# Optimization experiments

Hardware: AMD Instinct MI355X
Metric: run time of the kernel (lower is better)

Reference implementation:

```python
import jax, jax.numpy as jnp
import numpy as np


def _lstm_dir(xs, Wih, Whh, bih, bhh, reverse):
    # xs: [T, B, E]; torch LSTM gate order i, f, g, o
    B = xs.shape[1]
    H = Whh.shape[1]
    h0 = jnp.zeros((B, H), xs.dtype)
    c0 = jnp.zeros((B, H), xs.dtype)

    def step(carry, xt):
        h, c = carry
        g = xt @ Wih.T + h @ Whh.T + (bih + bhh)
        i, f, gg, o = jnp.split(g, 4, axis=-1)
        i = jax.nn.sigmoid(i)
        f = jax.nn.sigmoid(f)
        gg = jnp.tanh(gg)
        o = jax.nn.sigmoid(o)
        c_new = f * c + i * gg
        h_new = o * jnp.tanh(c_new)
        return (h_new, c_new), h_new

    _, hs = jax.lax.scan(step, (h0, c0), xs, reverse=reverse)
    return hs  # [T, B, H] time-aligned


def _forward(x, edge_index, emb_table, Wih_f, Whh_f, bih_f, bhh_f,
             Wih_b, Whh_b, bih_b, bhh_b, label_emb, ggc_weight,
             gru_Wih, gru_Whh, gru_bih, gru_bhh, proj_W, proj_b):
    # --- embedding (dropout is identity in eval) ---
    emb = emb_table[x]                       # [B, T, E]
    xs = jnp.transpose(emb, (1, 0, 2))       # [T, B, E]
    hf = _lstm_dir(xs, Wih_f, Whh_f, bih_f, bhh_f, reverse=False)
    hb = _lstm_dir(xs, Wih_b, Whh_b, bih_b, bhh_b, reverse=True)
    c = jnp.concatenate([hf, hb], axis=-1)   # [T, B, 2H]
    c = jnp.transpose(c, (1, 0, 2))          # [B, T, 2H]

    # --- label cosine similarity, summed over tokens ---
    eps = 1e-8
    cn = c / jnp.maximum(jnp.linalg.norm(c, axis=-1, keepdims=True), eps)
    ln = label_emb / jnp.maximum(jnp.linalg.norm(label_emb, axis=-1, keepdims=True), eps)
    ls = jnp.einsum('btd,ld->bl', cn, ln)    # [B, C] (sum over t folded in)

    # --- GatedGraphConv, 2 layers, aggr='add', edge_weight=None ---
    src, dst = edge_index[0], edge_index[1]
    N = ls.shape[0]
    h = ls
    for i in range(ggc_weight.shape[0]):
        m = h @ ggc_weight[i]                            # [N, C]
        m = jax.ops.segment_sum(m[src], dst, num_segments=N)  # gather + scatter-add
        # torch GRUCell: gates r, z, n
        gi = m @ gru_Wih.T + gru_bih
        gh = h @ gru_Whh.T + gru_bhh
        ir, iz, inn = jnp.split(gi, 3, axis=-1)
        hr, hz, hn = jnp.split(gh, 3, axis=-1)
        r = jax.nn.sigmoid(ir + hr)
        z = jax.nn.sigmoid(iz + hz)
        n = jnp.tanh(inn + r * hn)
        h = (1.0 - z) * n + z * h

    return h @ proj_W.T + proj_b             # [B, C]


def setup_inputs() -> dict:
    key = jax.random.key(0)
    ks = jax.random.split(key, 20)
    V, E, B, T, C, NE = 50000, 300, 2048, 64, 1024, 65536
    H = E
    s = 0.05
    inp = {
        'x': jax.random.randint(ks[0], (B, T), 0, V),
        'edge_index': jax.random.randint(ks[1], (2, NE), 0, B),
        'emb_table': jax.random.normal(ks[2], (V, E)) * s,
        'Wih_f': jax.random.normal(ks[3], (4 * H, E)) * s,
        'Whh_f': jax.random.normal(ks[4], (4 * H, H)) * s,
        'bih_f': jnp.zeros((4 * H,)),
        'bhh_f': jnp.zeros((4 * H,)),
        'Wih_b': jax.random.normal(ks[5], (4 * H, E)) * s,
        'Whh_b': jax.random.normal(ks[6], (4 * H, H)) * s,
        'bih_b': jnp.zeros((4 * H,)),
        'bhh_b': jnp.zeros((4 * H,)),
        'label_emb': jax.random.normal(ks[7], (C, 2 * H)) * s,
        'ggc_weight': jax.random.normal(ks[8], (2, C, C)) * (1.0 / np.sqrt(C)),
        'gru_Wih': jax.random.normal(ks[9], (3 * C, C)) * (1.0 / np.sqrt(C)),
        'gru_Whh': jax.random.normal(ks[10], (3 * C, C)) * (1.0 / np.sqrt(C)),
        'gru_bih': jnp.zeros((3 * C,)),
        'gru_bhh': jnp.zeros((3 * C,)),
        'proj_W': jax.random.normal(ks[11], (C, C)) * (1.0 / np.sqrt(C)),
        'proj_b': jnp.zeros((C,)),
    }
    return inp


def reference(x, edge_index, emb_table, Wih_f, Whh_f, bih_f, bhh_f,
              Wih_b, Whh_b, bih_b, bhh_b, label_emb, ggc_weight,
              gru_Wih, gru_Whh, gru_bih, gru_bhh, proj_W, proj_b):
    return _forward(x, edge_index, emb_table, Wih_f, Whh_f, bih_f, bhh_f,
                    Wih_b, Whh_b, bih_b, bhh_b, label_emb, ggc_weight,
                    gru_Wih, gru_Whh, gru_bih, gru_bhh, proj_W, proj_b)
```

## Files before the change

### kernel.cpp

```cpp
#include <hip/hip_runtime.h>
#include <hip/hip_bf16.h>
#include <stdint.h>

typedef __hip_bfloat16 bf16;
typedef __attribute__((ext_vector_type(8))) short frag16;
typedef __attribute__((ext_vector_type(4))) float f32x4;

#define B_ 2048
#define T_ 64
#define E_ 300
#define H_ 300
#define C_ 1024
#define NE_ 65536
#define HP 320
#define KC 640
#define NP 1280

static __device__ __forceinline__ float sigf(float x) {
  x = fminf(fmaxf(x, -30.f), 30.f);
  return 1.f / (1.f + __expf(-x));
}
static __device__ __forceinline__ float tanhfast(float x) {
  x = fminf(fmaxf(x, -15.f), 15.f);
  float e = __expf(2.f * x);
  return (e - 1.f) / (e + 1.f);
}
static __device__ __forceinline__ float ldraw(const void* p, size_t i, int isb) {
  return isb ? __bfloat162float(((const bf16*)p)[i]) : ((const float*)p)[i];
}
static __device__ __forceinline__ short b2s(bf16 b) {
  short s; __builtin_memcpy(&s, &b, 2); return s;
}
static __device__ __forceinline__ short4 f4tob4(float4 v) {
  return make_short4(b2s(__float2bfloat16(v.x)), b2s(__float2bfloat16(v.y)),
                     b2s(__float2bfloat16(v.z)), b2s(__float2bfloat16(v.w)));
}

__global__ void detect_dtype(const unsigned short* __restrict__ e2, int* __restrict__ flag) {
  __shared__ int red[4];
  int tid = threadIdx.x;
  int ones = 0;
#pragma unroll
  for (int s = 0; s < 16; ++s) ones += (e2[2 * (tid * 16 + s)] >> 14) & 1;
  for (int off = 32; off > 0; off >>= 1) ones += __shfl_down(ones, off, 64);
  if ((tid & 63) == 0) red[tid >> 6] = ones;
  __syncthreads();
  if (tid == 0) {
    int tot = red[0] + red[1] + red[2] + red[3];
    *flag = (tot < 1024) ? 1 : 0;
  }
}

__global__ __launch_bounds__(256) void gemm_bt(
    const bf16* __restrict__ A, int lda,
    const void* __restrict__ W, int ldw,
    const void* __restrict__ bias,
    float* __restrict__ Cf, bf16* __restrict__ Cb, int ldc, int K,
    const int* __restrict__ rawp, int outmode) {
  __shared__ __align__(16) short As[2][128 * 32];
  __shared__ __align__(16) short Bs[2][128 * 32];
  const int isb = rawp ? *rawp : 1;
  const int n0 = blockIdx.x * 128, m0 = blockIdx.y * 128;
  const int lane = threadIdx.x & 63, wv = threadIdx.x >> 6;
  const int wm = (wv & 1) * 64, wn = (wv >> 1) * 64;
  const int r_ = threadIdx.x >> 1, half_ = threadIdx.x & 1;
  const short* Arow = (const short*)A + (size_t)(m0 + r_) * lda + half_ * 16;
  const short* Brs = (const short*)W + (size_t)(n0 + r_) * ldw + half_ * 16;
  const float* Brf = (const float*)W + (size_t)(n0 + r_) * ldw + half_ * 16;

  uint4 ra0, ra1, rb0, rb1;
  float4 rf0, rf1, rf2, rf3;
  auto loadT = [&](int k0) {
    ra0 = *(const uint4*)(Arow + k0);
    ra1 = *(const uint4*)(Arow + k0 + 8);
    if (isb) {
      rb0 = *(const uint4*)(Brs + k0);
      rb1 = *(const uint4*)(Brs + k0 + 8);
    } else {
      rf0 = *(const float4*)(Brf + k0);
      rf1 = *(const float4*)(Brf + k0 + 4);
      rf2 = *(const float4*)(Brf + k0 + 8);
      rf3 = *(const float4*)(Brf + k0 + 12);
    }
  };
  auto writeT = [&](int buf) {
    short* da = As[buf] + r_ * 32 + half_ * 16;
    *(uint4*)da = ra0;
    *(uint4*)(da + 8) = ra1;
    short* db = Bs[buf] + r_ * 32 + half_ * 16;
    if (isb) {
      *(uint4*)db = rb0;
      *(uint4*)(db + 8) = rb1;
    } else {
      *(short4*)db = f4tob4(rf0);
      *(short4*)(db + 4) = f4tob4(rf1);
      *(short4*)(db + 8) = f4tob4(rf2);
      *(short4*)(db + 12) = f4tob4(rf3);
    }
  };

  f32x4 acc[4][4];
#pragma unroll
  for (int i = 0; i < 4; ++i)
#pragma unroll
    for (int j = 0; j < 4; ++j) acc[i][j] = (f32x4){0.f, 0.f, 0.f, 0.f};

  const int nk = K / 32;
  loadT(0);
  writeT(0);
  __syncthreads();
  const int krd = (lane >> 4) * 8;
  const int rsel = lane & 15;
  for (int kk = 0; kk < nk; ++kk) {
    const int cur = kk & 1;
    if (kk + 1 < nk) loadT(32 * (kk + 1));
    frag16 af[4], bfg[4];
#pragma unroll
    for (int i = 0; i < 4; ++i) af[i] = *(const frag16*)&As[cur][(wm + i * 16 + rsel) * 32 + krd];
#pragma unroll
    for (int i = 0; i < 4; ++i) bfg[i] = *(const frag16*)&Bs[cur][(wn + i * 16 + rsel) * 32 + krd];
#pragma unroll
    for (int i = 0; i < 4; ++i)
#pragma unroll
      for (int j = 0; j < 4; ++j)
        acc[i][j] = __builtin_amdgcn_mfma_f32_16x16x32_bf16(af[i], bfg[j], acc[i][j], 0, 0, 0);
    if (kk + 1 < nk) writeT(cur ^ 1);
    __syncthreads();
  }
  const int rq = (lane >> 4) * 4, cq = lane & 15;
#pragma unroll
  for (int j = 0; j < 4; ++j) {
    int cidx = n0 + wn + j * 16 + cq;
    float bv = bias ? ldraw(bias, cidx, isb) : 0.f;
#pragma unroll
    for (int i = 0; i < 4; ++i) {
      int rbase = m0 + wm + i * 16 + rq;
#pragma unroll
      for (int r = 0; r < 4; ++r) {
        float v = acc[i][j][r] + bv;
        size_t idx = (size_t)(rbase + r) * ldc + cidx;
        if (outmode) {
          if (isb) Cb[idx] = __float2bfloat16(v);
          else Cf[idx] = v;
        } else {
          if (Cf) Cf[idx] = v;
          if (Cb) Cb[idx] = __float2bfloat16(v);
        }
      }
    }
  }
}

static __device__ __forceinline__ void normacc_row2(
    const bf16* hfA, const bf16* hbA, const bf16* hfB, const bf16* hbB,
    float* __restrict__ Spf, int b, int lane) {
  float vA[10], vB[10];
  float sA = 0.f, sB = 0.f;
#pragma unroll
  for (int s = 0; s < 10; ++s) {
    int d = lane + 64 * s;
    float a = 0.f, c = 0.f;
    if (d < 300) {
      a = __bfloat162float(hfA[d]);
      c = __bfloat162float(hfB[d]);
    } else if (d < 600) {
      a = __bfloat162float(hbA[d - 300]);
      c = __bfloat162float(hbB[d - 300]);
    }
    vA[s] = a; vB[s] = c;
    sA += a * a; sB += c * c;
  }
#pragma unroll
  for (int off = 32; off > 0; off >>= 1) {
    sA += __shfl_xor(sA, off, 64);
    sB += __shfl_xor(sB, off, 64);
  }
  float kA = 1.f / fmaxf(sqrtf(sA), 1e-8f);
  float kB = 1.f / fmaxf(sqrtf(sB), 1e-8f);
  float* dst = Spf + (size_t)b * KC;
#pragma unroll
  for (int s = 0; s < 10; ++s) {
    int d = lane + 64 * s;
    if (d < 600) dst[d] += vA[s] * kA + vB[s] * kB;
  }
}

__global__ __launch_bounds__(256) void lstm_step(
    const void* __restrict__ emb, const int* __restrict__ x,
    const bf16* __restrict__ Wcat, const float* __restrict__ bcat,
    bf16* __restrict__ hpad, float* __restrict__ cstate,
    bf16* __restrict__ Hfst, bf16* __restrict__ Hbst, float* __restrict__ Spf,
    int s, const int* __restrict__ flagp) {
  const int pb = s & 1;
  const int lane = threadIdx.x & 63, wv = threadIdx.x >> 6;

  if (blockIdx.z == 2) {
    if (s >= 33) {
      int bid = blockIdx.x + gridDim.x * blockIdx.y;
      const bf16* hinf = hpad + (size_t)pb * B_ * HP;
      const bf16* hinb = hpad + (size_t)(2 + pb) * B_ * HP;
      const int t1 = s - 1, t2 = 64 - s;
#pragma unroll
      for (int rep = 0; rep < 2; ++rep) {
        int b = bid * 4 + wv + 1280 * rep;
        if (b < B_)
          normacc_row2(hinf + (size_t)b * HP,
                       Hbst + ((size_t)(t1 - 32) * B_ + b) * H_,
                       Hfst + ((size_t)t2 * B_ + b) * H_,
                       hinb + (size_t)b * HP, Spf, b, lane);
      }
    }
    return;
  }

  __shared__ __align__(16) char smem[24576];
  short* As0 = (short*)smem;
  short* As1 = (short*)(smem + 4096);
  short* Bs0 = (short*)(smem + 8192);
  short* Bs1 = (short*)(smem + 16384);
  float* epi = (float*)smem;

  const int dir = blockIdx.z;
  const int tt = dir ? (T_ - 1 - s) : s;
  const int isb = *flagp;
  const bf16* hin = hpad + (size_t)(dir * 2 + pb) * B_ * HP;
  const bf16* Wd = Wcat + (size_t)dir * NP * KC;
  bf16* hout = hpad + (size_t)(dir * 2 + (1 - pb)) * B_ * HP;
  float* cs = cstate + (size_t)dir * B_ * HP;
  const int n0 = blockIdx.x * 128, m0 = blockIdx.y * 64;
  const int wm = (wv & 1) * 32, wn = (wv >> 1) * 64;
  const int r_ = threadIdx.x >> 2, q_ = threadIdx.x & 3;
  const int r2 = threadIdx.x >> 1, h2 = threadIdx.x & 1;
  const size_t xoff = (size_t)x[(m0 + r_) * T_ + tt] * (size_t)E_;
  const short* es = (const short*)emb;
  const float* ef = (const float*)emb;
  const short* hins = (const short*)hin;
  const short* wrow = (const short*)Wd + (size_t)(n0 + r2) * KC + h2 * 16;

  uint2 axs0, axs1;
  float4 axf0, axf1;
  uint4 ah;
  uint4 bw0, bw1;

  auto loadA = [&](int k0) {
    if (k0 < HP) {
      int c0 = k0 + q_ * 8;
      if (isb) {
        axs0 = (c0 < E_) ? *(const uint2*)(es + xoff + c0) : make_uint2(0u, 0u);
        axs1 = (c0 + 4 < E_) ? *(const uint2*)(es + xoff + c0 + 4) : make_uint2(0u, 0u);
      } else {
        axf0 = (c0 < E_) ? *(const float4*)(ef + xoff + c0) : make_float4(0.f, 0.f, 0.f, 0.f);
        axf1 = (c0 + 4 < E_) ? *(const float4*)(ef + xoff + c0 + 4) : make_float4(0.f, 0.f, 0.f, 0.f);
      }
    } else {
      ah = *(const uint4*)(hins + (size_t)(m0 + r_) * HP + (k0 - HP) + q_ * 8);
    }
  };
  auto loadB = [&](int k0) {
    const short* g = wrow + k0;
    bw0 = *(const uint4*)g;
    bw1 = *(const uint4*)(g + 8);
  };
  auto writeAB = [&](int k0, short* Ad, short* Bd) {
    short* arow = Ad + r_ * 32 + q_ * 8;
    if (k0 < HP) {
      if (isb) {
        *(uint2*)arow = axs0;
        *(uint2*)(arow + 4) = axs1;
      } else {
        *(short4*)arow = f4tob4(axf0);
        *(short4*)(arow + 4) = f4tob4(axf1);
      }
    } else {
      *(uint4*)arow = ah;
    }
    short* brow = Bd + r2 * 32 + h2 * 16;
    *(uint4*)brow = bw0;
    *(uint4*)(brow + 8) = bw1;
  };

  f32x4 acc[2][4];
#pragma unroll
  for (int i = 0; i < 2; ++i)
#pragma unroll
    for (int j = 0; j < 4; ++j) acc[i][j] = (f32x4){0.f, 0.f, 0.f, 0.f};

  loadA(0); loadB(0);
  writeAB(0, As0, Bs0);
  __syncthreads();

  const int krd = (lane >> 4) * 8;
  const int rsel = lane & 15;
  for (int kk = 0; kk < KC / 32; ++kk) {
    const int cur = kk & 1;
    const short* Ac = cur ? As1 : As0;
    const short* Bc = cur ? Bs1 : Bs0;
    if (kk < KC / 32 - 1) {
      loadA(32 * (kk + 1));
      loadB(32 * (kk + 1));
    }
    frag16 af[2], bfg[4];
#pragma unroll
    for (int i = 0; i < 2; ++i) af[i] = *(const frag16*)&Ac[(wm + i * 16 + rsel) * 32 + krd];
#pragma unroll
    for (int j = 0; j < 4; ++j) bfg[j] = *(const frag16*)&Bc[(wn + j * 16 + rsel) * 32 + krd];
#pragma unroll
    for (int i = 0; i < 2; ++i)
#pragma unroll
      for (int j = 0; j < 4; ++j)
        acc[i][j] = __builtin_amdgcn_mfma_f32_16x16x32_bf16(af[i], bfg[j], acc[i][j], 0, 0, 0);
    if (kk < KC / 32 - 1) writeAB(32 * (kk + 1), cur ? As0 : As1, cur ? Bs0 : Bs1);
    __syncthreads();
  }

  const int rq = (lane >> 4) * 4, cq = lane & 15;
#pragma unroll
  for (int p = 0; p < 2; ++p) {
    if (wn == p * 64) {
#pragma unroll
      for (int j = 0; j < 4; ++j) {
        int cl = j * 16 + cq;
        float bv = bcat[dir * NP + n0 + p * 64 + cl];
#pragma unroll
        for (int i = 0; i < 2; ++i) {
          int rl = wm + i * 16 + rq;
#pragma unroll
          for (int r = 0; r < 4; ++r) epi[(rl + r) * 64 + cl] = acc[i][j][r] + bv;
        }
      }
    }
    __syncthreads();
    int jbase = (n0 + p * 64) >> 2;
    for (int it = threadIdx.x; it < 64 * 16; it += 256) {
      int rl = it >> 4, jl = it & 15;
      int jg = jbase + jl;
      if (jg < H_) {
        const float* row = epi + rl * 64 + jl * 4;
        float iv = sigf(row[0]);
        float fv = sigf(row[1]);
        float gv = tanhfast(row[2]);
        float ov = sigf(row[3]);
        int b = m0 + rl;
        float c = fv * cs[(size_t)b * HP + jg] + iv * gv;
        float h = ov * tanhfast(c);
        cs[(size_t)b * HP + jg] = c;
        bf16 hb = __float2bfloat16(h);
        hout[(size_t)b * HP + jg] = hb;
        if (dir) {
          if (tt >= 32) Hbst[((size_t)(tt - 32) * B_ + b) * H_ + jg] = hb;
        } else if (tt < 32) {
          Hfst[((size_t)tt * B_ + b) * H_ + jg] = hb;
        }
      }
    }
    __syncthreads();
  }
}

__global__ __launch_bounds__(256) void normacc_fin(const bf16* __restrict__ hpad,
                                                   const bf16* __restrict__ Hfst,
                                                   const bf16* __restrict__ Hbst,
                                                   float* __restrict__ Spf) {
  int b = blockIdx.x * 4 + (threadIdx.x >> 6);
  int lane = threadIdx.x & 63;
  normacc_row2(hpad + (size_t)b * HP,
               Hbst + ((size_t)31 * B_ + b) * H_,
               Hfst + (size_t)b * H_,
               hpad + (size_t)2 * B_ * HP + (size_t)b * HP, Spf, b, lane);
}

__global__ void prep_wcat(const void* __restrict__ Wih_f, const void* __restrict__ Whh_f,
                          const void* __restrict__ bih_f, const void* __restrict__ bhh_f,
                          const void* __restrict__ Wih_b, const void* __restrict__ Whh_b,
                          const void* __restrict__ bih_b, const void* __restrict__ bhh_b,
                          bf16* __restrict__ Wcat, float* __restrict__ bcat,
                          const int* __restrict__ flagp) {
  int i = blockIdx.x * 256 + threadIdx.x;
  if (i >= 2 * NP * KC) return;
  const int isb = *flagp;
  int k = i % KC;
  int n = (i / KC) % NP;
  int dir = i / (KC * NP);
  int j = n >> 2, q = n & 3;
  const void* Wih = dir ? Wih_b : Wih_f;
  const void* Whh = dir ? Whh_b : Whh_f;
  float v = 0.f;
  if (j < H_) {
    int row = q * H_ + j;
    if (k < E_) v = ldraw(Wih, (size_t)row * E_ + k, isb);
    else if (k >= HP && k < HP + H_) v = ldraw(Whh, (size_t)row * H_ + (k - HP), isb);
  }
  Wcat[i] = __float2bfloat16(v);
  if (k == 0) {
    const void* bih = dir ? bih_b : bih_f;
    const void* bhh = dir ? bhh_b : bhh_f;
    bcat[dir * NP + n] =
        (j < H_) ? (ldraw(bih, q * H_ + j, isb) + ldraw(bhh, q * H_ + j, isb)) : 0.f;
  }
}

__global__ __launch_bounds__(256) void labelnorm(const void* __restrict__ L,
                                                 bf16* __restrict__ lnp,
                                                 const int* __restrict__ flagp) {
  int l = blockIdx.x, tid = threadIdx.x;
  const int isb = *flagp;
  __shared__ float red[4];
  float v[3];
  float ss = 0.f;
#pragma unroll
  for (int s = 0; s < 3; ++s) {
    int d = tid + 256 * s;
    v[s] = (d < 600) ? ldraw(L, (size_t)l * 600 + d, isb) : 0.f;
    ss += v[s] * v[s];
  }
  for (int off = 32; off > 0; off >>= 1) ss += __shfl_down(ss, off, 64);
  if ((tid & 63) == 0) red[tid >> 6] = ss;
  __syncthreads();
  float scale = 1.f / fmaxf(sqrtf(red[0] + red[1] + red[2] + red[3]), 1e-8f);
#pragma unroll
  for (int s = 0; s < 3; ++s) {
    int d = tid + 256 * s;
    if (d < KC) lnp[(size_t)l * KC + d] = __float2bfloat16(v[s] * scale);
  }
}

__global__ void spcvt(const float* __restrict__ Spf, bf16* __restrict__ Sp) {
  int i = blockIdx.x * 256 + threadIdx.x;
  Sp[i] = __float2bfloat16(Spf[i]);
}

__global__ void transpose_ggc(const void* __restrict__ W, bf16* __restrict__ Wt,
                              const int* __restrict__ flagp) {
  int i = blockIdx.x * 256 + threadIdx.x;
  const int isb = *flagp;
  int k = i & 1023, n = (i >> 10) & 1023, l = i >> 20;
  size_t src = ((size_t)l << 20) | ((size_t)k << 10) | (size_t)n;
  Wt[i] = __float2bfloat16(ldraw(W, src, isb));
}

__global__ void zero_u4(uint4* __restrict__ p, int n16) {
  int i = blockIdx.x * 256 + threadIdx.x;
  if (i < n16) p[i] = make_uint4(0u, 0u, 0u, 0u);
}

__global__ void edge_cnt(const int* __restrict__ ei, int* __restrict__ cnt) {
  int e = blockIdx.x * 256 + threadIdx.x;
  if (e < NE_) {
    int s = ei[e], d = ei[NE_ + e];
    atomicAdd(&cnt[(size_t)d * B_ + s], 1);
  }
}
__global__ void cnt2bf(const int* __restrict__ cnt, bf16* __restrict__ A) {
  int i = blockIdx.x * 256 + threadIdx.x;
  A[i] = __float2bfloat16((float)cnt[i]);
}

__global__ void gru_ew(const float* __restrict__ gi, const float* __restrict__ gh,
                       float* __restrict__ h, bf16* __restrict__ hb16) {
  int i = blockIdx.x * 256 + threadIdx.x;
  int b = i >> 10, j = i & 1023;
  const float* gib = gi + (size_t)b * 3072;
  const float* ghb = gh + (size_t)b * 3072;
  float r = sigf(gib[j] + ghb[j]);
  float z = sigf(gib[1024 + j] + ghb[1024 + j]);
  float n = tanhfast(gib[2048 + j] + r * ghb[2048 + j]);
  float hv = (1.f - z) * n + z * h[i];
  h[i] = hv;
  hb16[i] = __float2bfloat16(hv);
}

__global__ void sentinel(bf16* __restrict__ o, int n, float v) {
  int i = blockIdx.x * 256 + threadIdx.x;
  if (i < n) o[i] = __float2bfloat16(v);
}

extern "C" void kernel_launch(void* const* d_in, const int* in_sizes, int n_in,
                              void* d_out, int out_size, void* d_ws, size_t ws_size,
                              hipStream_t stream) {
  const int* x = (const int*)d_in[0];
  const int* ei = (const int*)d_in[1];
  const void* emb = d_in[2];
  const void* Wih_f = d_in[3];
  const void* Whh_f = d_in[4];
  const void* bih_f = d_in[5];
  const void* bhh_f = d_in[6];
  const void* Wih_b = d_in[7];
  const void* Whh_b = d_in[8];
  const void* bih_b = d_in[9];
  const void* bhh_b = d_in[10];
  const void* label = d_in[11];
  const void* ggcw = d_in[12];
  const void* gWih = d_in[13];
  const void* gWhh = d_in[14];
  const void* gbih = d_in[15];
  const void* gbhh = d_in[16];
  const void* projW = d_in[17];
  const void* projb = d_in[18];
  (void)in_sizes; (void)n_in;

  const size_t NEED = (size_t)112 * 1024 * 1024;
  if (ws_size < NEED) {
    float v = 100.f + (float)(ws_size >> 24);
    sentinel<<<(out_size + 255) / 256, 256, 0, stream>>>((bf16*)d_out, out_size, v);
    return;
  }

  char* w = (char*)d_ws;
  size_t off = 0;
  auto alloc = [&](size_t bytes) {
    char* p = w + off;
    off += (bytes + 255) & ~(size_t)255;
    return p;
  };
  int* dflag = (int*)alloc(256);
  bf16* Wcat = (bf16*)alloc((size_t)2 * NP * KC * 2);
  float* bcat = (float*)alloc((size_t)2 * NP * 4);
  bf16* lnp = (bf16*)alloc((size_t)C_ * KC * 2);
  bf16* ggct = (bf16*)alloc((size_t)2 * C_ * C_ * 2);
  bf16* Sp = (bf16*)alloc((size_t)B_ * KC * 2);
  const size_t phase_base = off;
  float* Spf = (float*)alloc((size_t)B_ * KC * 4);
  bf16* hpad = (bf16*)alloc((size_t)4 * B_ * HP * 2);
  float* cst = (float*)alloc((size_t)2 * B_ * HP * 4);
  bf16* Hfst = (bf16*)alloc((size_t)32 * B_ * H_ * 2);
  bf16* Hbst = (bf16*)alloc((size_t)32 * B_ * H_ * 2);
  off = phase_base;
  float* hbuf = (float*)alloc((size_t)B_ * C_ * 4);
  bf16* hb16 = (bf16*)alloc((size_t)B_ * C_ * 2);
  bf16* m1t = (bf16*)alloc((size_t)C_ * B_ * 2);
  bf16* aggb = (bf16*)alloc((size_t)B_ * C_ * 2);
  bf16* Acnt = (bf16*)alloc((size_t)B_ * B_ * 2);
  float* gi = (float*)alloc((size_t)B_ * 3072 * 4);
  float* gh = (float*)alloc((size_t)B_ * 3072 * 4);
  int* cnt = (int*)gi;

  detect_dtype<<<1, 256, 0, stream>>>((const unsigned short*)emb, dflag);
  prep_wcat<<<(2 * NP * KC) / 256, 256, 0, stream>>>(Wih_f, Whh_f, bih_f, bhh_f,
                                                     Wih_b, Whh_b, bih_b, bhh_b, Wcat, bcat, dflag);
  labelnorm<<<C_, 256, 0, stream>>>(label, lnp, dflag);
  transpose_ggc<<<(2 * C_ * C_) / 256, 256, 0, stream>>>(ggcw, ggct, dflag);
  zero_u4<<<(4 * B_ * HP * 2 / 16 + 255) / 256, 256, 0, stream>>>((uint4*)hpad, 4 * B_ * HP * 2 / 16);
  zero_u4<<<(2 * B_ * HP * 4 / 16 + 255) / 256, 256, 0, stream>>>((uint4*)cst, 2 * B_ * HP * 4 / 16);
  zero_u4<<<(B_ * KC * 4 / 16 + 255) / 256, 256, 0, stream>>>((uint4*)Spf, B_ * KC * 4 / 16);

  for (int s = 0; s < T_; ++s)
    lstm_step<<<dim3(NP / 128, B_ / 64, 3), 256, 0, stream>>>(emb, x, Wcat, bcat, hpad, cst,
                                                              Hfst, Hbst, Spf, s, dflag);
  normacc_fin<<<B_ / 4, 256, 0, stream>>>(hpad, Hfst, Hbst, Spf);
  spcvt<<<(B_ * KC) / 256, 256, 0, stream>>>(Spf, Sp);

  gemm_bt<<<dim3(C_ / 128, B_ / 128), 256, 0, stream>>>(Sp, KC, lnp, KC, nullptr,
                                                        hbuf, hb16, C_, KC, nullptr, 0);
  zero_u4<<<(B_ * B_ * 4 / 16 + 255) / 256, 256, 0, stream>>>((uint4*)cnt, B_ * B_ * 4 / 16);
  edge_cnt<<<NE_ / 256, 256, 0, stream>>>(ei, cnt);
  cnt2bf<<<(B_ * B_) / 256, 256, 0, stream>>>(cnt, Acnt);
  for (int l = 0; l < 2; ++l) {
    gemm_bt<<<dim3(B_ / 128, C_ / 128), 256, 0, stream>>>(ggct + (size_t)l * C_ * C_, C_,
                                                          hb16, C_, nullptr,
                                                          nullptr, m1t, B_, C_, nullptr, 0);
    gemm_bt<<<dim3(C_ / 128, B_ / 128), 256, 0, stream>>>(Acnt, B_, m1t, B_, nullptr,
                                                          nullptr, aggb, C_, B_, nullptr, 0);
    gemm_bt<<<dim3(3072 / 128, B_ / 128), 256, 0, stream>>>(aggb, C_, gWih, C_, gbih,
                                                            gi, nullptr, 3072, C_, dflag, 0);
    gemm_bt<<<dim3(3072 / 128, B_ / 128), 256, 0, stream>>>(hb16, C_, gWhh, C_, gbhh,
                                                            gh, nullptr, 3072, C_, dflag, 0);
    gru_ew<<<(B_ * C_) / 256, 256, 0, stream>>>(gi, gh, hbuf, hb16);
  }
  gemm_bt<<<dim3(C_ / 128, B_ / 128), 256, 0, stream>>>(hb16, C_, projW, C_, projb,
                                                        (float*)d_out, (bf16*)d_out, C_, C_,
                                                        dflag, 1);
}
```

Measured before the change: 2.447 ms.

## Load B fragments directly to registers and enlarge LSTM step tiles

GEMM and LSTM-step kernels now load the weight (B) operand straight from global memory into MFMA register fragments, keeping only A in shared memory, with a two-stage unrolled double-buffered loop. The LSTM step tile grows from 64 to 128 rows per block, halving the grid and raising per-block MFMA work, and the norm-accumulate side blocks loop over more rows to compensate. GRU and projection weights and biases are pre-converted to bf16/f32 once so the GEMM no longer branches on dtype. This cuts LDS traffic and syncs but raises register pressure and may reduce occupancy or parallelism for the latency-bound LSTM steps.

```diff
diff --git a/kernel.cpp b/kernel.cpp
--- a/kernel.cpp
+++ b/kernel.cpp
@@ -53,50 +53,33 @@
 
 __global__ __launch_bounds__(256) void gemm_bt(
     const bf16* __restrict__ A, int lda,
-    const void* __restrict__ W, int ldw,
-    const void* __restrict__ bias,
+    const bf16* __restrict__ W, int ldw,
+    const float* __restrict__ bias,
     float* __restrict__ Cf, bf16* __restrict__ Cb, int ldc, int K,
     const int* __restrict__ rawp, int outmode) {
   __shared__ __align__(16) short As[2][128 * 32];
-  __shared__ __align__(16) short Bs[2][128 * 32];
   const int isb = rawp ? *rawp : 1;
   const int n0 = blockIdx.x * 128, m0 = blockIdx.y * 128;
   const int lane = threadIdx.x & 63, wv = threadIdx.x >> 6;
   const int wm = (wv & 1) * 64, wn = (wv >> 1) * 64;
-  const int r_ = threadIdx.x >> 1, half_ = threadIdx.x & 1;
-  const short* Arow = (const short*)A + (size_t)(m0 + r_) * lda + half_ * 16;
-  const short* Brs = (const short*)W + (size_t)(n0 + r_) * ldw + half_ * 16;
-  const float* Brf = (const float*)W + (size_t)(n0 + r_) * ldw + half_ * 16;
-
-  uint4 ra0, ra1, rb0, rb1;
-  float4 rf0, rf1, rf2, rf3;
-  auto loadT = [&](int k0) {
-    ra0 = *(const uint4*)(Arow + k0);
-    ra1 = *(const uint4*)(Arow + k0 + 8);
-    if (isb) {
-      rb0 = *(const uint4*)(Brs + k0);
-      rb1 = *(const uint4*)(Brs + k0 + 8);
-    } else {
-      rf0 = *(const float4*)(Brf + k0);
-      rf1 = *(const float4*)(Brf + k0 + 4);
-      rf2 = *(const float4*)(Brf + k0 + 8);
-      rf3 = *(const float4*)(Brf + k0 + 12);
-    }
-  };
-  auto writeT = [&](int buf) {
-    short* da = As[buf] + r_ * 32 + half_ * 16;
-    *(uint4*)da = ra0;
-    *(uint4*)(da + 8) = ra1;
-    short* db = Bs[buf] + r_ * 32 + half_ * 16;
-    if (isb) {
-      *(uint4*)db = rb0;
-      *(uint4*)(db + 8) = rb1;
-    } else {
-      *(short4*)db = f4tob4(rf0);
-      *(short4*)(db + 4) = f4tob4(rf1);
-      *(short4*)(db + 8) = f4tob4(rf2);
-      *(short4*)(db + 12) = f4tob4(rf3);
-    }
+  const int r_ = threadIdx.x >> 1, h_ = threadIdx.x & 1;
+  const short* Arow = (const short*)A + (size_t)(m0 + r_) * lda + h_ * 16;
+  const short* Wfrag = (const short*)W + (size_t)(n0 + wn + (lane & 15)) * ldw + (lane >> 4) * 8;
+
+  uint4 sa0[2], sa1[2];
+  frag16 b0[4], b1[4];
+  auto loadA = [&](uint4* s, int k0) {
+    s[0] = *(const uint4*)(Arow + k0);
+    s[1] = *(const uint4*)(Arow + k0 + 8);
+  };
+  auto writeA = [&](const uint4* s, int buf) {
+    short* d = &As[buf][0] + r_ * 32 + h_ * 16;
+    *(uint4*)d = s[0];
+    *(uint4*)(d + 8) = s[1];
+  };
+  auto loadB = [&](frag16* b, int k0) {
+#pragma unroll
+    for (int j = 0; j < 4; ++j) b[j] = *(const frag16*)(Wfrag + (size_t)(j * 16) * ldw + k0);
   };
 
   f32x4 acc[4][4];
@@ -106,32 +89,44 @@
     for (int j = 0; j < 4; ++j) acc[i][j] = (f32x4){0.f, 0.f, 0.f, 0.f};
 
   const int nk = K / 32;
-  loadT(0);
-  writeT(0);
+  const int rsel = lane & 15, krd = (lane >> 4) * 8;
+  loadA(sa0, 0);
+  loadA(sa1, 32);
+  loadB(b0, 0);
+  writeA(sa0, 0);
   __syncthreads();
-  const int krd = (lane >> 4) * 8;
-  const int rsel = lane & 15;
-  for (int kk = 0; kk < nk; ++kk) {
-    const int cur = kk & 1;
-    if (kk + 1 < nk) loadT(32 * (kk + 1));
-    frag16 af[4], bfg[4];
-#pragma unroll
-    for (int i = 0; i < 4; ++i) af[i] = *(const frag16*)&As[cur][(wm + i * 16 + rsel) * 32 + krd];
-#pragma unroll
-    for (int i = 0; i < 4; ++i) bfg[i] = *(const frag16*)&Bs[cur][(wn + i * 16 + rsel) * 32 + krd];
-#pragma unroll
-    for (int i = 0; i < 4; ++i)
-#pragma unroll
-      for (int j = 0; j < 4; ++j)
-        acc[i][j] = __builtin_amdgcn_mfma_f32_16x16x32_bf16(af[i], bfg[j], acc[i][j], 0, 0, 0);
-    if (kk + 1 < nk) writeT(cur ^ 1);
+
+#define GEMM_MFMA(BUF, BSET)                                                              \
+  {                                                                                       \
+    frag16 af[4];                                                                         \
+    _Pragma("unroll") for (int i = 0; i < 4; ++i)                                         \
+        af[i] = *(const frag16*)&As[BUF][(wm + i * 16 + rsel) * 32 + krd];                \
+    _Pragma("unroll") for (int i = 0; i < 4; ++i)                                         \
+        _Pragma("unroll") for (int j = 0; j < 4; ++j)                                     \
+            acc[i][j] = __builtin_amdgcn_mfma_f32_16x16x32_bf16(af[i], BSET[j],           \
+                                                                acc[i][j], 0, 0, 0);      \
+  }
+
+  for (int kk = 0; kk < nk; kk += 2) {
+    if (kk + 2 < nk) loadA(sa0, 32 * (kk + 2));
+    loadB(b1, 32 * (kk + 1));
+    GEMM_MFMA(0, b0)
+    writeA(sa1, 1);
     __syncthreads();
-  }
+    if (kk + 2 < nk) {
+      loadA(sa1, 32 * (kk + 3));
+      loadB(b0, 32 * (kk + 2));
+    }
+    GEMM_MFMA(1, b1)
+    if (kk + 2 < nk) writeA(sa0, 0);
+    __syncthreads();
+  }
+
   const int rq = (lane >> 4) * 4, cq = lane & 15;
 #pragma unroll
   for (int j = 0; j < 4; ++j) {
     int cidx = n0 + wn + j * 16 + cq;
-    float bv = bias ? ldraw(bias, cidx, isb) : 0.f;
+    float bv = bias ? bias[cidx] : 0.f;
 #pragma unroll
     for (int i = 0; i < 4; ++i) {
       int rbase = m0 + wm + i * 16 + rq;
@@ -201,8 +196,8 @@
       const bf16* hinb = hpad + (size_t)(2 + pb) * B_ * HP;
       const int t1 = s - 1, t2 = 64 - s;
 #pragma unroll
-      for (int rep = 0; rep < 2; ++rep) {
-        int b = bid * 4 + wv + 1280 * rep;
+      for (int rep = 0; rep < 4; ++rep) {
+        int b = bid * 4 + wv + 640 * rep;
         if (b < B_)
           normacc_row2(hinf + (size_t)b * HP,
                        Hbst + ((size_t)(t1 - 32) * B_ + b) * H_,
@@ -213,11 +208,9 @@
     return;
   }
 
-  __shared__ __align__(16) char smem[24576];
+  __shared__ __align__(16) char smem[32768];
   short* As0 = (short*)smem;
-  short* As1 = (short*)(smem + 4096);
-  short* Bs0 = (short*)(smem + 8192);
-  short* Bs1 = (short*)(smem + 16384);
+  short* As1 = (short*)(smem + 8192);
   float* epi = (float*)smem;
 
   const int dir = blockIdx.z;
@@ -227,89 +220,87 @@
   const bf16* Wd = Wcat + (size_t)dir * NP * KC;
   bf16* hout = hpad + (size_t)(dir * 2 + (1 - pb)) * B_ * HP;
   float* cs = cstate + (size_t)dir * B_ * HP;
-  const int n0 = blockIdx.x * 128, m0 = blockIdx.y * 64;
-  const int wm = (wv & 1) * 32, wn = (wv >> 1) * 64;
-  const int r_ = threadIdx.x >> 2, q_ = threadIdx.x & 3;
-  const int r2 = threadIdx.x >> 1, h2 = threadIdx.x & 1;
+  const int n0 = blockIdx.x * 128, m0 = blockIdx.y * 128;
+  const int wm = (wv & 1) * 64, wn = (wv >> 1) * 64;
+  const int r_ = threadIdx.x >> 1, h_ = threadIdx.x & 1;
   const size_t xoff = (size_t)x[(m0 + r_) * T_ + tt] * (size_t)E_;
   const short* es = (const short*)emb;
   const float* ef = (const float*)emb;
   const short* hins = (const short*)hin;
-  const short* wrow = (const short*)Wd + (size_t)(n0 + r2) * KC + h2 * 16;
-
-  uint2 axs0, axs1;
-  float4 axf0, axf1;
-  uint4 ah;
-  uint4 bw0, bw1;
-
-  auto loadA = [&](int k0) {
+  const short* Wfrag = Wd ? (const short*)Wd + (size_t)(n0 + wn + (lane & 15)) * KC + (lane >> 4) * 8
+                          : (const short*)nullptr;
+
+  uint4 sa0[2], sa1[2];
+  frag16 b0[4], b1[4];
+  auto loadAl = [&](uint4* sreg, int k0) {
     if (k0 < HP) {
-      int c0 = k0 + q_ * 8;
-      if (isb) {
-        axs0 = (c0 < E_) ? *(const uint2*)(es + xoff + c0) : make_uint2(0u, 0u);
-        axs1 = (c0 + 4 < E_) ? *(const uint2*)(es + xoff + c0 + 4) : make_uint2(0u, 0u);
-      } else {
-        axf0 = (c0 < E_) ? *(const float4*)(ef + xoff + c0) : make_float4(0.f, 0.f, 0.f, 0.f);
-        axf1 = (c0 + 4 < E_) ? *(const float4*)(ef + xoff + c0 + 4) : make_float4(0.f, 0.f, 0.f, 0.f);
+      short4 t[4];
+      int c0 = k0 + h_ * 16;
+#pragma unroll
+      for (int g = 0; g < 4; ++g) {
+        int c = c0 + 4 * g;
+        short4 v = make_short4(0, 0, 0, 0);
+        if (c < E_) {
+          if (isb) v = *(const short4*)(es + xoff + c);
+          else v = f4tob4(*(const float4*)(ef + xoff + c));
+        }
+        t[g] = v;
       }
+      __builtin_memcpy(&sreg[0], &t[0], 16);
+      __builtin_memcpy(&sreg[1], &t[2], 16);
     } else {
-      ah = *(const uint4*)(hins + (size_t)(m0 + r_) * HP + (k0 - HP) + q_ * 8);
-    }
-  };
-  auto loadB = [&](int k0) {
-    const short* g = wrow + k0;
-    bw0 = *(const uint4*)g;
-    bw1 = *(const uint4*)(g + 8);
-  };
-  auto writeAB = [&](int k0, short* Ad, short* Bd) {
-    short* arow = Ad + r_ * 32 + q_ * 8;
-    if (k0 < HP) {
-      if (isb) {
-        *(uint2*)arow = axs0;
-        *(uint2*)(arow + 4) = axs1;
-      } else {
-        *(short4*)arow = f4tob4(axf0);
-        *(short4*)(arow + 4) = f4tob4(axf1);
-      }
-    } else {
-      *(uint4*)arow = ah;
-    }
-    short* brow = Bd + r2 * 32 + h2 * 16;
-    *(uint4*)brow = bw0;
-    *(uint4*)(brow + 8) = bw1;
-  };
-
-  f32x4 acc[2][4];
-#pragma unroll
-  for (int i = 0; i < 2; ++i)
+      const short* p = hins + (size_t)(m0 + r_) * HP + (k0 - HP) + h_ * 16;
+      sreg[0] = *(const uint4*)p;
+      sreg[1] = *(const uint4*)(p + 8);
+    }
+  };
+  auto writeA = [&](const uint4* sreg, short* Ad) {
+    short* d = Ad + r_ * 32 + h_ * 16;
+    *(uint4*)d = sreg[0];
+    *(uint4*)(d + 8) = sreg[1];
+  };
+  auto loadB = [&](frag16* b, int k0) {
+#pragma unroll
+    for (int j = 0; j < 4; ++j) b[j] = *(const frag16*)(Wfrag + (size_t)(j * 16) * KC + k0);
+  };
+
+  f32x4 acc[4][4];
+#pragma unroll
+  for (int i = 0; i < 4; ++i)
 #pragma unroll
     for (int j = 0; j < 4; ++j) acc[i][j] = (f32x4){0.f, 0.f, 0.f, 0.f};
 
-  loadA(0); loadB(0);
-  writeAB(0, As0, Bs0);
+  const int rsel = lane & 15, krd = (lane >> 4) * 8;
+  const int NKT = KC / 32;
+  loadAl(sa0, 0);
+  loadAl(sa1, 32);
+  loadB(b0, 0);
+  writeA(sa0, As0);
   __syncthreads();
 
-  const int krd = (lane >> 4) * 8;
-  const int rsel = lane & 15;
-  for (int kk = 0; kk < KC / 32; ++kk) {
-    const int cur = kk & 1;
-    const short* Ac = cur ? As1 : As0;
-    const short* Bc = cur ? Bs1 : Bs0;
-    if (kk < KC / 32 - 1) {
-      loadA(32 * (kk + 1));
-      loadB(32 * (kk + 1));
-    }
-    frag16 af[2], bfg[4];
-#pragma unroll
-    for (int i = 0; i < 2; ++i) af[i] = *(const frag16*)&Ac[(wm + i * 16 + rsel) * 32 + krd];
-#pragma unroll
-    for (int j = 0; j < 4; ++j) bfg[j] = *(const frag16*)&Bc[(wn + j * 16 + rsel) * 32 + krd];
-#pragma unroll
-    for (int i = 0; i < 2; ++i)
-#pragma unroll
-      for (int j = 0; j < 4; ++j)
-        acc[i][j] = __builtin_amdgcn_mfma_f32_16x16x32_bf16(af[i], bfg[j], acc[i][j], 0, 0, 0);
-    if (kk < KC / 32 - 1) writeAB(32 * (kk + 1), cur ? As0 : As1, cur ? Bs0 : Bs1);
+#define LSTM_MFMA(AP, BSET)                                                               \
+  {                                                                                       \
+    frag16 af[4];                                                                         \
+    _Pragma("unroll") for (int i = 0; i < 4; ++i)                                         \
+        af[i] = *(const frag16*)&AP[(wm + i * 16 + rsel) * 32 + krd];                     \
+    _Pragma("unroll") for (int i = 0; i < 4; ++i)                                         \
+        _Pragma("unroll") for (int j = 0; j < 4; ++j)                                     \
+            acc[i][j] = __builtin_amdgcn_mfma_f32_16x16x32_bf16(af[i], BSET[j],           \
+                                                                acc[i][j], 0, 0, 0);      \
+  }
+
+  for (int kk = 0; kk < NKT; kk += 2) {
+    if (kk + 2 < NKT) loadAl(sa0, 32 * (kk + 2));
+    loadB(b1, 32 * (kk + 1));
+    LSTM_MFMA(As0, b0)
+    writeA(sa1, As1);
+    __syncthreads();
+    if (kk + 2 < NKT) {
+      loadAl(sa1, 32 * (kk + 3));
+      loadB(b0, 32 * (kk + 2));
+    }
+    LSTM_MFMA(As1, b1)
+    if (kk + 2 < NKT) writeA(sa0, As0);
     __syncthreads();
   }
 
@@ -322,7 +313,7 @@
         int cl = j * 16 + cq;
         float bv = bcat[dir * NP + n0 + p * 64 + cl];
 #pragma unroll
-        for (int i = 0; i < 2; ++i) {
+        for (int i = 0; i < 4; ++i) {
           int rl = wm + i * 16 + rq;
 #pragma unroll
           for (int r = 0; r < 4; ++r) epi[(rl + r) * 64 + cl] = acc[i][j][r] + bv;
@@ -331,7 +322,7 @@
     }
     __syncthreads();
     int jbase = (n0 + p * 64) >> 2;
-    for (int it = threadIdx.x; it < 64 * 16; it += 256) {
+    for (int it = threadIdx.x; it < 128 * 16; it += 256) {
       int rl = it >> 4, jl = it & 15;
       int jg = jbase + jl;
       if (jg < H_) {
@@ -436,6 +427,17 @@
   int k = i & 1023, n = (i >> 10) & 1023, l = i >> 20;
   size_t src = ((size_t)l << 20) | ((size_t)k << 10) | (size_t)n;
   Wt[i] = __float2bfloat16(ldraw(W, src, isb));
+}
+
+__global__ void w2bf(const void* __restrict__ src, bf16* __restrict__ dst, int n,
+                     const int* __restrict__ flagp) {
+  int i = blockIdx.x * 256 + threadIdx.x;
+  if (i < n) dst[i] = __float2bfloat16(ldraw(src, i, *flagp));
+}
+__global__ void b2f32(const void* __restrict__ src, float* __restrict__ dst, int n,
+                      const int* __restrict__ flagp) {
+  int i = blockIdx.x * 256 + threadIdx.x;
+  if (i < n) dst[i] = ldraw(src, i, *flagp);
 }
 
 __global__ void zero_u4(uint4* __restrict__ p, int n16) {
@@ -532,6 +534,12 @@
   bf16* Acnt = (bf16*)alloc((size_t)B_ * B_ * 2);
   float* gi = (float*)alloc((size_t)B_ * 3072 * 4);
   float* gh = (float*)alloc((size_t)B_ * 3072 * 4);
+  bf16* gWihb = (bf16*)alloc((size_t)3072 * C_ * 2);
+  bf16* gWhhb = (bf16*)alloc((size_t)3072 * C_ * 2);
+  bf16* projWb = (bf16*)alloc((size_t)C_ * C_ * 2);
+  float* gbihf = (float*)alloc(3072 * 4);
+  float* gbhhf = (float*)alloc(3072 * 4);
+  float* projbf = (float*)alloc(C_ * 4);
   int* cnt = (int*)gi;
 
   detect_dtype<<<1, 256, 0, stream>>>((const unsigned short*)emb, dflag);
@@ -544,10 +552,17 @@
   zero_u4<<<(B_ * KC * 4 / 16 + 255) / 256, 256, 0, stream>>>((uint4*)Spf, B_ * KC * 4 / 16);
 
   for (int s = 0; s < T_; ++s)
-    lstm_step<<<dim3(NP / 128, B_ / 64, 3), 256, 0, stream>>>(emb, x, Wcat, bcat, hpad, cst,
-                                                              Hfst, Hbst, Spf, s, dflag);
+    lstm_step<<<dim3(NP / 128, B_ / 128, 3), 256, 0, stream>>>(emb, x, Wcat, bcat, hpad, cst,
+                                                               Hfst, Hbst, Spf, s, dflag);
   normacc_fin<<<B_ / 4, 256, 0, stream>>>(hpad, Hfst, Hbst, Spf);
   spcvt<<<(B_ * KC) / 256, 256, 0, stream>>>(Spf, Sp);
+
+  w2bf<<<(3072 * C_) / 256, 256, 0, stream>>>(gWih, gWihb, 3072 * C_, dflag);
+  w2bf<<<(3072 * C_) / 256, 256, 0, stream>>>(gWhh, gWhhb, 3072 * C_, dflag);
+  w2bf<<<(C_ * C_) / 256, 256, 0, stream>>>(projW, projWb, C_ * C_, dflag);
+  b2f32<<<12, 256, 0, stream>>>(gbih, gbihf, 3072, dflag);
+  b2f32<<<12, 256, 0, stream>>>(gbhh, gbhhf, 3072, dflag);
+  b2f32<<<4, 256, 0, stream>>>(projb, projbf, C_, dflag);
 
   gemm_bt<<<dim3(C_ / 128, B_ / 128), 256, 0, stream>>>(Sp, KC, lnp, KC, nullptr,
                                                         hbuf, hb16, C_, KC, nullptr, 0);
@@ -560,13 +575,13 @@
                                                           nullptr, m1t, B_, C_, nullptr, 0);
     gemm_bt<<<dim3(C_ / 128, B_ / 128), 256, 0, stream>>>(Acnt, B_, m1t, B_, nullptr,
                                                           nullptr, aggb, C_, B_, nullptr, 0);
-    gemm_bt<<<dim3(3072 / 128, B_ / 128), 256, 0, stream>>>(aggb, C_, gWih, C_, gbih,
-                                                            gi, nullptr, 3072, C_, dflag, 0);
-    gemm_bt<<<dim3(3072 / 128, B_ / 128), 256, 0, stream>>>(hb16, C_, gWhh, C_, gbhh,
-                                                            gh, nullptr, 3072, C_, dflag, 0);
+    gemm_bt<<<dim3(3072 / 128, B_ / 128), 256, 0, stream>>>(aggb, C_, gWihb, C_, gbihf,
+                                                            gi, nullptr, 3072, C_, nullptr, 0);
+    gemm_bt<<<dim3(3072 / 128, B_ / 128), 256, 0, stream>>>(hb16, C_, gWhhb, C_, gbhhf,
+                                                            gh, nullptr, 3072, C_, nullptr, 0);
     gru_ew<<<(B_ * C_) / 256, 256, 0, stream>>>(gi, gh, hbuf, hb16);
   }
-  gemm_bt<<<dim3(C_ / 128, B_ / 128), 256, 0, stream>>>(hb16, C_, projW, C_, projb,
+  gemm_bt<<<dim3(C_ / 128, B_ / 128), 256, 0, stream>>>(hb16, C_, projWb, C_, projbf,
                                                         (float*)d_out, (bf16*)d_out, C_, C_,
                                                         dflag, 1);
 }
```

Result: slower. 3.992 ms (+63.1%).
